# Performance work log

Measured on AMD Instinct MI355X. Metric: run time of the kernel, lower is better.

The kernel has to match this reference:

```python
import jax, jax.numpy as jnp
import numpy as np

N_NODES = 100000
N_EDGES = 1600000


def _lin_init(k, din, dout):
    # xavier-normal-ish weight, zero bias handled separately
    s = (2.0 / (din + dout)) ** 0.5
    return jax.random.normal(k, (din, dout), jnp.float32) * s


def setup_inputs() -> dict:
    key = jax.random.key(0)
    ks = jax.random.split(key, 32)
    inp = {
        "node_feat": jax.random.normal(ks[0], (N_NODES, 3), jnp.float32),
        "edge_feat": jax.random.normal(ks[1], (N_EDGES, 1), jnp.float32),
        "edge_dist": jax.random.normal(ks[2], (N_EDGES, 1), jnp.float32),
        "src": jax.random.randint(ks[3], (N_EDGES,), 0, N_NODES),
        "dst": jax.random.randint(ks[4], (N_EDGES,), 0, N_NODES),
    }
    dims = {"enc": [3, 64, 64, 8], "dec": [8, 64, 64, 1],
            "nod": [9, 64, 64, 8], "edg": [17, 64, 64, 1]}
    i = 5
    for name, d in dims.items():
        for l in range(3):
            inp[f"w_{name}{l+1}"] = _lin_init(ks[i], d[l], d[l + 1]); i += 1
            inp[f"b_{name}{l+1}"] = jnp.zeros((d[l + 1],), jnp.float32)
    return inp


def _mlp(x, w1, b1, w2, b2, w3, b3):
    x = jax.nn.relu(x @ w1 + b1)
    x = jax.nn.relu(x @ w2 + b2)
    return jax.nn.relu(x @ w3 + b3)


def _edge_softmax(dist, dst, n):
    # softmax over incoming edges per destination node (DGL edge_softmax)
    m = jax.ops.segment_max(dist, dst, num_segments=n)          # [N,1]
    e = jnp.exp(dist - m[dst])                                   # [E,1]
    s = jax.ops.segment_sum(e, dst, num_segments=n)              # [N,1]
    return e / s[dst]


def reference(node_feat, edge_feat, edge_dist, src, dst,
              w_enc1, b_enc1, w_enc2, b_enc2, w_enc3, b_enc3,
              w_dec1, b_dec1, w_dec2, b_dec2, w_dec3, b_dec3,
              w_nod1, b_nod1, w_nod2, b_nod2, w_nod3, b_nod3,
              w_edg1, b_edg1, w_edg2, b_edg2, w_edg3, b_edg3):
    n = node_feat.shape[0]
    # encoder: [N,3] -> [N,8]
    h = _mlp(node_feat, w_enc1, b_enc1, w_enc2, b_enc2, w_enc3, b_enc3)
    # softmax-weighted aggregation of src features to dst
    w = _edge_softmax(edge_dist, dst, n)                         # [E,1]
    h = jax.ops.segment_sum(w * h[src], dst, num_segments=n)     # [N,8]
    he = edge_feat                                               # [E,1]
    for _ in range(2):
        x = jnp.concatenate([he, h[src], h[dst]], axis=-1)       # [E,17]
        he = _mlp(x, w_edg1, b_edg1, w_edg2, b_edg2, w_edg3, b_edg3)  # [E,1]
        agg = jax.ops.segment_sum(he, dst, num_segments=n)       # [N,1]
        h = _mlp(jnp.concatenate([agg, h], axis=-1),
                 w_nod1, b_nod1, w_nod2, b_nod2, w_nod3, b_nod3)  # [N,8]
    # second softmax aggregation (same dist -> same weights)
    h = jax.ops.segment_sum(w * h[src], dst, num_segments=n)     # [N,8]
    # decoder: [N,8] -> [N,1]
    return _mlp(h, w_dec1, b_dec1, w_dec2, b_dec2, w_dec3, b_dec3)
```

## Files before the change

### kernel.cpp

```cpp
#include <hip/hip_runtime.h>

#define N_NODES 100000
#define N_EDGES 1600000

typedef __attribute__((ext_vector_type(4))) float f32x4;
typedef __attribute__((ext_vector_type(8))) short bf16x8;

__device__ __forceinline__ unsigned short f2bf(float v) {
    unsigned u = __float_as_uint(v);
    unsigned r = (u + 0x7FFFu + ((u >> 16) & 1u)) >> 16;
    return (unsigned short)r;
}
__device__ __forceinline__ float bf2f(unsigned short h) {
    return __uint_as_float(((unsigned)h) << 16);
}

__global__ void zero_kernel(float* p, int n) {
    int i = blockIdx.x * blockDim.x + threadIdx.x;
    int stride = gridDim.x * blockDim.x;
    for (; i < n; i += stride) p[i] = 0.f;
}

__global__ void exp_sum_kernel(const float* __restrict__ dist, const int* __restrict__ dst,
                               float* __restrict__ s, float* __restrict__ wbuf, int E) {
    int e = blockIdx.x * blockDim.x + threadIdx.x;
    if (e >= E) return;
    float v = expf(dist[e]);
    wbuf[e] = v;
    atomicAdd(s + dst[e], v);
}

template <bool NORM>
__global__ void agg_kernel(float* wbuf, const float* __restrict__ s,
                           const float* __restrict__ hfeat,
                           const int* __restrict__ src, const int* __restrict__ dst,
                           float* __restrict__ out, int E) {
    int t = blockIdx.x * blockDim.x + threadIdx.x;
    if (t >= E * 8) return;
    int e = t >> 3, c = t & 7;
    float w = wbuf[e];
    int d = dst[e];
    if (NORM) {
        w = w / s[d];
        if (c == 0) wbuf[e] = w;
    }
    atomicAdd(out + d * 8 + c, w * hfeat[src[e] * 8 + c]);
}

struct PackArgs { const float *w1, *b1, *w2; float* out; int din, stride; };

__global__ void pack_kernel(PackArgs a0, PackArgs a1, PackArgs a2) {
    PackArgs a = (blockIdx.x == 0) ? a0 : (blockIdx.x == 1) ? a1 : a2;
    int k = threadIdx.x;
    float* row = a.out + k * a.stride;
    for (int j = 0; j < 64; ++j) row[j] = a.w2[k * 64 + j];
    for (int j = 0; j < a.din; ++j) row[64 + j] = a.w1[j * 64 + k];
    row[64 + a.din] = a.b1[k];
}

__global__ void pack_edge_kernel(const float* __restrict__ w1, const float* __restrict__ w2,
                                 unsigned short* __restrict__ w1hi, unsigned short* __restrict__ w1lo,
                                 unsigned short* __restrict__ w2hi, unsigned short* __restrict__ w2lo) {
    int c = threadIdx.x;
    for (int j = 0; j < 32; ++j) {
        float v = (j < 17) ? w1[j * 64 + c] : 0.f;
        unsigned short hi = f2bf(v);
        w1hi[c * 32 + j] = hi;
        w1lo[c * 32 + j] = f2bf(v - bf2f(hi));
    }
    int mt = c >> 4, row = c & 15;
    for (int ch = 0; ch < 64; ++ch) {
        int ks = ch >> 5, r5 = ch & 31;
        int i = ((r5 >> 4) << 2) | (r5 & 3);
        int g = (r5 >> 2) & 3;
        int dstIdx = (((mt * 2 + ks) * 16 + row) * 4 + g) * 8 + i;
        float v = w2[ch * 64 + c];
        unsigned short hi = f2bf(v);
        w2hi[dstIdx] = hi;
        w2lo[dstIdx] = f2bf(v - bf2f(hi));
    }
}

template <int DIN, int DOUT, int STRIDE>
__device__ __forceinline__ void mlp_fused(
    const float* __restrict__ x, const float* __restrict__ wp,
    const float* __restrict__ b2,
    const float* __restrict__ w3, const float* __restrict__ b3,
    float* __restrict__ out) {
    float h2[64];
#pragma unroll
    for (int j = 0; j < 64; ++j) h2[j] = b2[j];
    for (int k = 0; k < 64; ++k) {
        const float* row = wp + k * STRIDE;
        float a = row[64 + DIN];
#pragma unroll
        for (int j = 0; j < DIN; ++j) a = fmaf(x[j], row[64 + j], a);
        a = fmaxf(a, 0.f);
#pragma unroll
        for (int j = 0; j < 64; ++j) h2[j] = fmaf(a, row[j], h2[j]);
    }
    float acc[DOUT];
#pragma unroll
    for (int o = 0; o < DOUT; ++o) acc[o] = b3[o];
#pragma unroll
    for (int j = 0; j < 64; ++j) {
        float r = fmaxf(h2[j], 0.f);
#pragma unroll
        for (int o = 0; o < DOUT; ++o) acc[o] = fmaf(r, w3[j * DOUT + o], acc[o]);
    }
#pragma unroll
    for (int o = 0; o < DOUT; ++o) out[o] = fmaxf(acc[o], 0.f);
}

template <int CA, int CB, int DOUT, int STRIDE>
__global__ __launch_bounds__(256, 3) void node_mlp_kernel(
    const float* __restrict__ xa, const float* __restrict__ xb,
    const float* __restrict__ wp, const float* __restrict__ b2,
    const float* __restrict__ w3, const float* __restrict__ b3,
    float* __restrict__ out, int n) {
    constexpr int DIN = CA + CB;
    int i = blockIdx.x * 256 + threadIdx.x;
    if (i >= n) return;
    float x[DIN];
#pragma unroll
    for (int k = 0; k < CA; ++k) x[k] = xa[i * CA + k];
    if (CB == 8) {
        float4 v0 = *(const float4*)(xb + i * 8);
        float4 v1 = *(const float4*)(xb + i * 8 + 4);
        x[CA + 0] = v0.x; x[CA + 1] = v0.y; x[CA + 2] = v0.z; x[CA + 3] = v0.w;
        x[CA + 4] = v1.x; x[CA + 5] = v1.y; x[CA + 6] = v1.z; x[CA + 7] = v1.w;
    }
    float o[DOUT];
    mlp_fused<DIN, DOUT, STRIDE>(x, wp, b2, w3, b3, o);
#pragma unroll
    for (int k = 0; k < DOUT; ++k) out[i * DOUT + k] = o[k];
}

__global__ __launch_bounds__(128, 2) void edge_mlp_mfma_kernel(
    const float* __restrict__ he_in, const float* __restrict__ h,
    const int* __restrict__ src, const int* __restrict__ dst,
    const unsigned short* __restrict__ w1hi, const unsigned short* __restrict__ w1lo,
    const unsigned short* __restrict__ w2hi, const unsigned short* __restrict__ w2lo,
    const float* __restrict__ b1, const float* __restrict__ b2,
    const float* __restrict__ w3, const float* __restrict__ b3,
    float* __restrict__ he_out, float* __restrict__ agg) {
    __shared__ __align__(16) unsigned char smem[2 * 10240];
    const int lane = threadIdx.x & 63, wv = threadIdx.x >> 6;
    unsigned char* W = smem + wv * 10240;
    const int ebase = (blockIdx.x * 2 + wv) * 64;

    {
        int e = ebase + lane;
        float x[32];
        x[0] = he_in[e];
        int sr = src[e], dd = dst[e];
        float4 a0 = *(const float4*)(h + sr * 8);
        float4 a1 = *(const float4*)(h + sr * 8 + 4);
        float4 d0 = *(const float4*)(h + dd * 8);
        float4 d1 = *(const float4*)(h + dd * 8 + 4);
        x[1] = a0.x;  x[2] = a0.y;  x[3] = a0.z;  x[4] = a0.w;
        x[5] = a1.x;  x[6] = a1.y;  x[7] = a1.z;  x[8] = a1.w;
        x[9] = d0.x;  x[10] = d0.y; x[11] = d0.z; x[12] = d0.w;
        x[13] = d1.x; x[14] = d1.y; x[15] = d1.z; x[16] = d1.w;
#pragma unroll
        for (int j = 17; j < 32; ++j) x[j] = 0.f;
        unsigned uh[16], ul[16];
#pragma unroll
        for (int jj = 0; jj < 16; ++jj) {
            unsigned short h0 = f2bf(x[2 * jj]);
            unsigned short h1v = f2bf(x[2 * jj + 1]);
            unsigned short l0 = f2bf(x[2 * jj] - bf2f(h0));
            unsigned short l1 = f2bf(x[2 * jj + 1] - bf2f(h1v));
            uh[jj] = (unsigned)h0 | ((unsigned)h1v << 16);
            ul[jj] = (unsigned)l0 | ((unsigned)l1 << 16);
        }
        uint4* ph = (uint4*)(W + lane * 80);
        uint4* pl = (uint4*)(W + 5120 + lane * 80);
#pragma unroll
        for (int q = 0; q < 4; ++q) {
            ph[q] = make_uint4(uh[4 * q], uh[4 * q + 1], uh[4 * q + 2], uh[4 * q + 3]);
            pl[q] = make_uint4(ul[4 * q], ul[4 * q + 1], ul[4 * q + 2], ul[4 * q + 3]);
        }
    }
    __syncthreads();
    const int row = lane & 15, g = lane >> 4;

    bf16x8 wa_h[4], wa_l[4];
#pragma unroll
    for (int mt = 0; mt < 4; ++mt) {
        wa_h[mt] = *(const bf16x8*)(w1hi + (16 * mt + row) * 32 + g * 8);
        wa_l[mt] = *(const bf16x8*)(w1lo + (16 * mt + row) * 32 + g * 8);
    }
    bf16x8 xb_h[4], xb_l[4];
#pragma unroll
    for (int nt = 0; nt < 4; ++nt) {
        xb_h[nt] = *(const bf16x8*)(W + (16 * nt + row) * 80 + g * 16);
        xb_l[nt] = *(const bf16x8*)(W + 5120 + (16 * nt + row) * 80 + g * 16);
    }
    f32x4 c1[4][4];
#pragma unroll
    for (int mt = 0; mt < 4; ++mt)
#pragma unroll
        for (int nt = 0; nt < 4; ++nt) {
            f32x4 c = {0.f, 0.f, 0.f, 0.f};
            c = __builtin_amdgcn_mfma_f32_16x16x32_bf16(wa_h[mt], xb_h[nt], c, 0, 0, 0);
            c = __builtin_amdgcn_mfma_f32_16x16x32_bf16(wa_h[mt], xb_l[nt], c, 0, 0, 0);
            c = __builtin_amdgcn_mfma_f32_16x16x32_bf16(wa_l[mt], xb_h[nt], c, 0, 0, 0);
            c1[mt][nt] = c;
        }

    float4 b1v[4];
#pragma unroll
    for (int mt = 0; mt < 4; ++mt) b1v[mt] = *(const float4*)(b1 + 16 * mt + g * 4);
    bf16x8 pb_h[4][2], pb_l[4][2];
#pragma unroll
    for (int nt = 0; nt < 4; ++nt)
#pragma unroll
        for (int ks = 0; ks < 2; ++ks) {
            float v0 = fmaxf(c1[2 * ks][nt].x + b1v[2 * ks].x, 0.f);
            float v1 = fmaxf(c1[2 * ks][nt].y + b1v[2 * ks].y, 0.f);
            float v2 = fmaxf(c1[2 * ks][nt].z + b1v[2 * ks].z, 0.f);
            float v3 = fmaxf(c1[2 * ks][nt].w + b1v[2 * ks].w, 0.f);
            float v4 = fmaxf(c1[2 * ks + 1][nt].x + b1v[2 * ks + 1].x, 0.f);
            float v5 = fmaxf(c1[2 * ks + 1][nt].y + b1v[2 * ks + 1].y, 0.f);
            float v6 = fmaxf(c1[2 * ks + 1][nt].z + b1v[2 * ks + 1].z, 0.f);
            float v7 = fmaxf(c1[2 * ks + 1][nt].w + b1v[2 * ks + 1].w, 0.f);
            unsigned short h0 = f2bf(v0), h1v = f2bf(v1), h2v = f2bf(v2), h3 = f2bf(v3);
            unsigned short h4 = f2bf(v4), h5 = f2bf(v5), h6 = f2bf(v6), h7 = f2bf(v7);
            bf16x8 ph, pl;
            ph[0] = h0; ph[1] = h1v; ph[2] = h2v; ph[3] = h3;
            ph[4] = h4; ph[5] = h5;  ph[6] = h6;  ph[7] = h7;
            pl[0] = f2bf(v0 - bf2f(h0)); pl[1] = f2bf(v1 - bf2f(h1v));
            pl[2] = f2bf(v2 - bf2f(h2v)); pl[3] = f2bf(v3 - bf2f(h3));
            pl[4] = f2bf(v4 - bf2f(h4)); pl[5] = f2bf(v5 - bf2f(h5));
            pl[6] = f2bf(v6 - bf2f(h6)); pl[7] = f2bf(v7 - bf2f(h7));
            pb_h[nt][ks] = ph;
            pb_l[nt][ks] = pl;
        }

    f32x4 c2[4][4];
#pragma unroll
    for (int mt = 0; mt < 4; ++mt)
#pragma unroll
        for (int nt = 0; nt < 4; ++nt) c2[mt][nt] = (f32x4){0.f, 0.f, 0.f, 0.f};
#pragma unroll
    for (int mt = 0; mt < 4; ++mt) {
        bf16x8 w2a_h[2], w2a_l[2];
#pragma unroll
        for (int ks = 0; ks < 2; ++ks) {
            int off = (((mt * 2 + ks) * 16 + row) * 4 + g) * 8;
            w2a_h[ks] = *(const bf16x8*)(w2hi + off);
            w2a_l[ks] = *(const bf16x8*)(w2lo + off);
        }
#pragma unroll
        for (int nt = 0; nt < 4; ++nt)
#pragma unroll
            for (int ks = 0; ks < 2; ++ks) {
                c2[mt][nt] = __builtin_amdgcn_mfma_f32_16x16x32_bf16(w2a_h[ks], pb_h[nt][ks], c2[mt][nt], 0, 0, 0);
                c2[mt][nt] = __builtin_amdgcn_mfma_f32_16x16x32_bf16(w2a_h[ks], pb_l[nt][ks], c2[mt][nt], 0, 0, 0);
                c2[mt][nt] = __builtin_amdgcn_mfma_f32_16x16x32_bf16(w2a_l[ks], pb_h[nt][ks], c2[mt][nt], 0, 0, 0);
            }
    }

    float4 b2v[4], w3v[4];
#pragma unroll
    for (int mt = 0; mt < 4; ++mt) {
        b2v[mt] = *(const float4*)(b2 + 16 * mt + g * 4);
        w3v[mt] = *(const float4*)(w3 + 16 * mt + g * 4);
    }
    float b3s = b3[0];
    float pacc[4];
#pragma unroll
    for (int nt = 0; nt < 4; ++nt) {
        float p = 0.f;
#pragma unroll
        for (int mt = 0; mt < 4; ++mt) {
            p = fmaf(fmaxf(c2[mt][nt].x + b2v[mt].x, 0.f), w3v[mt].x, p);
            p = fmaf(fmaxf(c2[mt][nt].y + b2v[mt].y, 0.f), w3v[mt].y, p);
            p = fmaf(fmaxf(c2[mt][nt].z + b2v[mt].z, 0.f), w3v[mt].z, p);
            p = fmaf(fmaxf(c2[mt][nt].w + b2v[mt].w, 0.f), w3v[mt].w, p);
        }
        p += __shfl_xor(p, 16);
        p += __shfl_xor(p, 32);
        pacc[nt] = p;
    }
    if (lane < 16) {
#pragma unroll
        for (int nt = 0; nt < 4; ++nt) {
            int e2 = ebase + 16 * nt + lane;
            float o = fmaxf(pacc[nt] + b3s, 0.f);
            he_out[e2] = o;
            atomicAdd(agg + dst[e2], o);
        }
    }
}

extern "C" void kernel_launch(void* const* d_in, const int* in_sizes, int n_in,
                              void* d_out, int out_size, void* d_ws, size_t ws_size,
                              hipStream_t stream) {
    const int N = N_NODES, E = N_EDGES;
    const float* node_feat = (const float*)d_in[0];
    const float* edge_feat = (const float*)d_in[1];
    const float* edge_dist = (const float*)d_in[2];
    const int* src = (const int*)d_in[3];
    const int* dst = (const int*)d_in[4];
    const float* w_enc1 = (const float*)d_in[5];  const float* b_enc1 = (const float*)d_in[6];
    const float* w_enc2 = (const float*)d_in[7];  const float* b_enc2 = (const float*)d_in[8];
    const float* w_enc3 = (const float*)d_in[9];  const float* b_enc3 = (const float*)d_in[10];
    const float* w_dec1 = (const float*)d_in[11]; const float* b_dec1 = (const float*)d_in[12];
    const float* w_dec2 = (const float*)d_in[13]; const float* b_dec2 = (const float*)d_in[14];
    const float* w_dec3 = (const float*)d_in[15]; const float* b_dec3 = (const float*)d_in[16];
    const float* w_nod1 = (const float*)d_in[17]; const float* b_nod1 = (const float*)d_in[18];
    const float* w_nod2 = (const float*)d_in[19]; const float* b_nod2 = (const float*)d_in[20];
    const float* w_nod3 = (const float*)d_in[21]; const float* b_nod3 = (const float*)d_in[22];
    const float* w_edg1 = (const float*)d_in[23]; const float* b_edg1 = (const float*)d_in[24];
    const float* w_edg2 = (const float*)d_in[25]; const float* b_edg2 = (const float*)d_in[26];
    const float* w_edg3 = (const float*)d_in[27]; const float* b_edg3 = (const float*)d_in[28];

    float* ws = (float*)d_ws;
    float* s      = ws;
    float* hagg1  = ws + N;
    float* agg1   = ws + 9 * N;
    float* agg2   = ws + 10 * N;
    float* hagg2  = ws + 11 * N;
    float* h_enc  = ws + 19 * N;
    float* h_r1   = ws + 27 * N;
    float* h_r2   = ws + 35 * N;
    float* wbuf   = ws + 43 * N;
    float* he1    = wbuf + E;
    float* he2    = he1 + E;
    float* pk_enc = he2 + E;
    float* pk_nod = pk_enc + 64 * 80;
    float* pk_dec = pk_nod + 64 * 80;
    unsigned short* w1hi = (unsigned short*)(pk_dec + 64 * 80);
    unsigned short* w1lo = w1hi + 64 * 32;
    unsigned short* w2hi = w1lo + 64 * 32;
    unsigned short* w2lo = w2hi + 64 * 64;

    PackArgs pa0{w_enc1, b_enc1, w_enc2, pk_enc, 3, 80};
    PackArgs pa1{w_nod1, b_nod1, w_nod2, pk_nod, 9, 80};
    PackArgs pa2{w_dec1, b_dec1, w_dec2, pk_dec, 8, 80};
    pack_kernel<<<3, 64, 0, stream>>>(pa0, pa1, pa2);
    pack_edge_kernel<<<1, 64, 0, stream>>>(w_edg1, w_edg2, w1hi, w1lo, w2hi, w2lo);

    zero_kernel<<<2048, 256, 0, stream>>>(ws, 19 * N);
    node_mlp_kernel<3, 0, 8, 80><<<(N + 255) / 256, 256, 0, stream>>>(node_feat, nullptr,
        pk_enc, b_enc2, w_enc3, b_enc3, h_enc, N);
    exp_sum_kernel<<<(E + 255) / 256, 256, 0, stream>>>(edge_dist, dst, s, wbuf, E);
    agg_kernel<true><<<(E * 8 + 255) / 256, 256, 0, stream>>>(wbuf, s, h_enc, src, dst, hagg1, E);
    edge_mlp_mfma_kernel<<<E / 128, 128, 0, stream>>>(edge_feat, hagg1, src, dst,
        w1hi, w1lo, w2hi, w2lo, b_edg1, b_edg2, w_edg3, b_edg3, he1, agg1);
    node_mlp_kernel<1, 8, 8, 80><<<(N + 255) / 256, 256, 0, stream>>>(agg1, hagg1,
        pk_nod, b_nod2, w_nod3, b_nod3, h_r1, N);
    edge_mlp_mfma_kernel<<<E / 128, 128, 0, stream>>>(he1, h_r1, src, dst,
        w1hi, w1lo, w2hi, w2lo, b_edg1, b_edg2, w_edg3, b_edg3, he2, agg2);
    node_mlp_kernel<1, 8, 8, 80><<<(N + 255) / 256, 256, 0, stream>>>(agg2, h_r1,
        pk_nod, b_nod2, w_nod3, b_nod3, h_r2, N);
    agg_kernel<false><<<(E * 8 + 255) / 256, 256, 0, stream>>>(wbuf, s, h_r2, src, dst, hagg2, E);
    node_mlp_kernel<8, 0, 1, 80><<<(N + 255) / 256, 256, 0, stream>>>(hagg2, nullptr,
        pk_dec, b_dec2, w_dec3, b_dec3, (float*)d_out, N);
}
```

Baseline: 721.4 us.

## Build edge MLP B-fragments directly in registers, skipping LDS staging

The edge MLP kernel no longer gathers each edge's 17-feature input into shared memory and reads it back as MFMA fragments. Each lane now gathers its own 8-wide slice (src features, dst features, or the edge scalar) straight into bf16 hi/lo fragment registers. The first-layer weight packing is permuted to match this K ordering. The block grows to 4 waves of 256 threads with no LDS or barrier, and f2bf switches to the HIP intrinsic. The cost is more redundant gather loads per lane, since each edge row is loaded across four nt iterations by different lane groups, and possibly higher register pressure.

```diff
diff --git a/kernel.cpp b/kernel.cpp
--- a/kernel.cpp
+++ b/kernel.cpp
@@ -1,4 +1,5 @@
 #include <hip/hip_runtime.h>
+#include <hip/hip_bf16.h>
 
 #define N_NODES 100000
 #define N_EDGES 1600000
@@ -7,9 +8,7 @@
 typedef __attribute__((ext_vector_type(8))) short bf16x8;
 
 __device__ __forceinline__ unsigned short f2bf(float v) {
-    unsigned u = __float_as_uint(v);
-    unsigned r = (u + 0x7FFFu + ((u >> 16) & 1u)) >> 16;
-    return (unsigned short)r;
+    return __builtin_bit_cast(unsigned short, __float2bfloat16(v));
 }
 __device__ __forceinline__ float bf2f(unsigned short h) {
     return __uint_as_float(((unsigned)h) << 16);
@@ -62,11 +61,11 @@
                                  unsigned short* __restrict__ w1hi, unsigned short* __restrict__ w1lo,
                                  unsigned short* __restrict__ w2hi, unsigned short* __restrict__ w2lo) {
     int c = threadIdx.x;
-    for (int j = 0; j < 32; ++j) {
-        float v = (j < 17) ? w1[j * 64 + c] : 0.f;
+    for (int k = 0; k < 32; ++k) {
+        float v = (k < 16) ? w1[(k + 1) * 64 + c] : (k == 16 ? w1[c] : 0.f);
         unsigned short hi = f2bf(v);
-        w1hi[c * 32 + j] = hi;
-        w1lo[c * 32 + j] = f2bf(v - bf2f(hi));
+        w1hi[c * 32 + k] = hi;
+        w1lo[c * 32 + k] = f2bf(v - bf2f(hi));
     }
     int mt = c >> 4, row = c & 15;
     for (int ch = 0; ch < 64; ++ch) {
@@ -136,7 +135,7 @@
     for (int k = 0; k < DOUT; ++k) out[i * DOUT + k] = o[k];
 }
 
-__global__ __launch_bounds__(128, 2) void edge_mlp_mfma_kernel(
+__global__ __launch_bounds__(256) void edge_mlp_mfma_kernel(
     const float* __restrict__ he_in, const float* __restrict__ h,
     const int* __restrict__ src, const int* __restrict__ dst,
     const unsigned short* __restrict__ w1hi, const unsigned short* __restrict__ w1lo,
@@ -144,58 +143,42 @@
     const float* __restrict__ b1, const float* __restrict__ b2,
     const float* __restrict__ w3, const float* __restrict__ b3,
     float* __restrict__ he_out, float* __restrict__ agg) {
-    __shared__ __align__(16) unsigned char smem[2 * 10240];
     const int lane = threadIdx.x & 63, wv = threadIdx.x >> 6;
-    unsigned char* W = smem + wv * 10240;
-    const int ebase = (blockIdx.x * 2 + wv) * 64;
-
-    {
-        int e = ebase + lane;
-        float x[32];
-        x[0] = he_in[e];
-        int sr = src[e], dd = dst[e];
-        float4 a0 = *(const float4*)(h + sr * 8);
-        float4 a1 = *(const float4*)(h + sr * 8 + 4);
-        float4 d0 = *(const float4*)(h + dd * 8);
-        float4 d1 = *(const float4*)(h + dd * 8 + 4);
-        x[1] = a0.x;  x[2] = a0.y;  x[3] = a0.z;  x[4] = a0.w;
-        x[5] = a1.x;  x[6] = a1.y;  x[7] = a1.z;  x[8] = a1.w;
-        x[9] = d0.x;  x[10] = d0.y; x[11] = d0.z; x[12] = d0.w;
-        x[13] = d1.x; x[14] = d1.y; x[15] = d1.z; x[16] = d1.w;
-#pragma unroll
-        for (int j = 17; j < 32; ++j) x[j] = 0.f;
-        unsigned uh[16], ul[16];
-#pragma unroll
-        for (int jj = 0; jj < 16; ++jj) {
-            unsigned short h0 = f2bf(x[2 * jj]);
-            unsigned short h1v = f2bf(x[2 * jj + 1]);
-            unsigned short l0 = f2bf(x[2 * jj] - bf2f(h0));
-            unsigned short l1 = f2bf(x[2 * jj + 1] - bf2f(h1v));
-            uh[jj] = (unsigned)h0 | ((unsigned)h1v << 16);
-            ul[jj] = (unsigned)l0 | ((unsigned)l1 << 16);
-        }
-        uint4* ph = (uint4*)(W + lane * 80);
-        uint4* pl = (uint4*)(W + 5120 + lane * 80);
-#pragma unroll
-        for (int q = 0; q < 4; ++q) {
-            ph[q] = make_uint4(uh[4 * q], uh[4 * q + 1], uh[4 * q + 2], uh[4 * q + 3]);
-            pl[q] = make_uint4(ul[4 * q], ul[4 * q + 1], ul[4 * q + 2], ul[4 * q + 3]);
-        }
-    }
-    __syncthreads();
+    const int ebase = (blockIdx.x * 4 + wv) * 64;
     const int row = lane & 15, g = lane >> 4;
+
+    bf16x8 xb_h[4], xb_l[4];
+#pragma unroll
+    for (int nt = 0; nt < 4; ++nt) {
+        int e = ebase + 16 * nt + row;
+        float v[8];
+        if (g < 2) {
+            int n = (g == 0) ? src[e] : dst[e];
+            float4 A = *(const float4*)(h + n * 8);
+            float4 B = *(const float4*)(h + n * 8 + 4);
+            v[0] = A.x; v[1] = A.y; v[2] = A.z; v[3] = A.w;
+            v[4] = B.x; v[5] = B.y; v[6] = B.z; v[7] = B.w;
+        } else {
+            v[0] = (g == 2) ? he_in[e] : 0.f;
+            v[1] = 0.f; v[2] = 0.f; v[3] = 0.f;
+            v[4] = 0.f; v[5] = 0.f; v[6] = 0.f; v[7] = 0.f;
+        }
+        bf16x8 hv, lv;
+#pragma unroll
+        for (int j = 0; j < 8; ++j) {
+            unsigned short hb = f2bf(v[j]);
+            hv[j] = (short)hb;
+            lv[j] = (short)f2bf(v[j] - bf2f(hb));
+        }
+        xb_h[nt] = hv;
+        xb_l[nt] = lv;
+    }
 
     bf16x8 wa_h[4], wa_l[4];
 #pragma unroll
     for (int mt = 0; mt < 4; ++mt) {
         wa_h[mt] = *(const bf16x8*)(w1hi + (16 * mt + row) * 32 + g * 8);
         wa_l[mt] = *(const bf16x8*)(w1lo + (16 * mt + row) * 32 + g * 8);
-    }
-    bf16x8 xb_h[4], xb_l[4];
-#pragma unroll
-    for (int nt = 0; nt < 4; ++nt) {
-        xb_h[nt] = *(const bf16x8*)(W + (16 * nt + row) * 80 + g * 16);
-        xb_l[nt] = *(const bf16x8*)(W + 5120 + (16 * nt + row) * 80 + g * 16);
     }
     f32x4 c1[4][4];
 #pragma unroll
@@ -348,11 +331,11 @@
         pk_enc, b_enc2, w_enc3, b_enc3, h_enc, N);
     exp_sum_kernel<<<(E + 255) / 256, 256, 0, stream>>>(edge_dist, dst, s, wbuf, E);
     agg_kernel<true><<<(E * 8 + 255) / 256, 256, 0, stream>>>(wbuf, s, h_enc, src, dst, hagg1, E);
-    edge_mlp_mfma_kernel<<<E / 128, 128, 0, stream>>>(edge_feat, hagg1, src, dst,
+    edge_mlp_mfma_kernel<<<E / 256, 256, 0, stream>>>(edge_feat, hagg1, src, dst,
         w1hi, w1lo, w2hi, w2lo, b_edg1, b_edg2, w_edg3, b_edg3, he1, agg1);
     node_mlp_kernel<1, 8, 8, 80><<<(N + 255) / 256, 256, 0, stream>>>(agg1, hagg1,
         pk_nod, b_nod2, w_nod3, b_nod3, h_r1, N);
-    edge_mlp_mfma_kernel<<<E / 128, 128, 0, stream>>>(he1, h_r1, src, dst,
+    edge_mlp_mfma_kernel<<<E / 256, 256, 0, stream>>>(he1, h_r1, src, dst,
         w1hi, w1lo, w2hi, w2lo, b_edg1, b_edg2, w_edg3, b_edg3, he2, agg2);
     node_mlp_kernel<1, 8, 8, 80><<<(N + 255) / 256, 256, 0, stream>>>(agg2, h_r1,
         pk_nod, b_nod2, w_nod3, b_nod3, h_r2, N);
```

New measurement: 751.8 us. 1.04x slower.

## Fuse edge softmax with first aggregation and defer normalization to per-node scale

Applied to the files above, without the earlier changes.

Merges the exp/sum pass and the first weighted aggregation into one per-edge kernel that accumulates unnormalized exp-weighted features. The softmax division moves to a per-node normalization pass, and for the second aggregation to a scale applied when the decoder loads its input. This drops one full edge pass and the per-edge division, and replaces 8-threads-per-edge gathers with one thread per edge doing float4 loads. The trade is more atomics issued per thread. Skipping the max subtraction was already the case before, so overflow risk is unchanged. The bf16 conversion helper also switches to the library intrinsic.

```diff
diff --git a/kernel.cpp b/kernel.cpp
--- a/kernel.cpp
+++ b/kernel.cpp
@@ -1,4 +1,5 @@
 #include <hip/hip_runtime.h>
+#include <hip/hip_bf16.h>
 
 #define N_NODES 100000
 #define N_EDGES 1600000
@@ -7,9 +8,7 @@
 typedef __attribute__((ext_vector_type(8))) short bf16x8;
 
 __device__ __forceinline__ unsigned short f2bf(float v) {
-    unsigned u = __float_as_uint(v);
-    unsigned r = (u + 0x7FFFu + ((u >> 16) & 1u)) >> 16;
-    return (unsigned short)r;
+    return __builtin_bit_cast(unsigned short, __float2bfloat16(v));
 }
 __device__ __forceinline__ float bf2f(unsigned short h) {
     return __uint_as_float(((unsigned)h) << 16);
@@ -21,30 +20,54 @@
     for (; i < n; i += stride) p[i] = 0.f;
 }
 
-__global__ void exp_sum_kernel(const float* __restrict__ dist, const int* __restrict__ dst,
-                               float* __restrict__ s, float* __restrict__ wbuf, int E) {
+__global__ void exp_agg_kernel(const float* __restrict__ dist,
+                               const int* __restrict__ src, const int* __restrict__ dst,
+                               const float* __restrict__ h,
+                               float* __restrict__ s, float* __restrict__ wbuf,
+                               float* __restrict__ hagg, int E) {
     int e = blockIdx.x * blockDim.x + threadIdx.x;
     if (e >= E) return;
     float v = expf(dist[e]);
     wbuf[e] = v;
-    atomicAdd(s + dst[e], v);
-}
-
-template <bool NORM>
-__global__ void agg_kernel(float* wbuf, const float* __restrict__ s,
-                           const float* __restrict__ hfeat,
-                           const int* __restrict__ src, const int* __restrict__ dst,
-                           float* __restrict__ out, int E) {
-    int t = blockIdx.x * blockDim.x + threadIdx.x;
-    if (t >= E * 8) return;
-    int e = t >> 3, c = t & 7;
-    float w = wbuf[e];
-    int d = dst[e];
-    if (NORM) {
-        w = w / s[d];
-        if (c == 0) wbuf[e] = w;
-    }
-    atomicAdd(out + d * 8 + c, w * hfeat[src[e] * 8 + c]);
+    int d = dst[e], sr = src[e];
+    atomicAdd(s + d, v);
+    float4 A = *(const float4*)(h + sr * 8);
+    float4 B = *(const float4*)(h + sr * 8 + 4);
+    float* o = hagg + d * 8;
+    atomicAdd(o + 0, v * A.x); atomicAdd(o + 1, v * A.y);
+    atomicAdd(o + 2, v * A.z); atomicAdd(o + 3, v * A.w);
+    atomicAdd(o + 4, v * B.x); atomicAdd(o + 5, v * B.y);
+    atomicAdd(o + 6, v * B.z); atomicAdd(o + 7, v * B.w);
+}
+
+__global__ void agg2_kernel(const float* __restrict__ wbuf, const float* __restrict__ h,
+                            const int* __restrict__ src, const int* __restrict__ dst,
+                            float* __restrict__ out, int E) {
+    int e = blockIdx.x * blockDim.x + threadIdx.x;
+    if (e >= E) return;
+    float v = wbuf[e];
+    int d = dst[e], sr = src[e];
+    float4 A = *(const float4*)(h + sr * 8);
+    float4 B = *(const float4*)(h + sr * 8 + 4);
+    float* o = out + d * 8;
+    atomicAdd(o + 0, v * A.x); atomicAdd(o + 1, v * A.y);
+    atomicAdd(o + 2, v * A.z); atomicAdd(o + 3, v * A.w);
+    atomicAdd(o + 4, v * B.x); atomicAdd(o + 5, v * B.y);
+    atomicAdd(o + 6, v * B.z); atomicAdd(o + 7, v * B.w);
+}
+
+__global__ void norm_kernel(float* __restrict__ hagg, const float* __restrict__ s,
+                            float* __restrict__ rs, int N) {
+    int d = blockIdx.x * blockDim.x + threadIdx.x;
+    if (d >= N) return;
+    float r = 1.f / s[d];
+    rs[d] = r;
+    float4 a = *(const float4*)(hagg + d * 8);
+    float4 b = *(const float4*)(hagg + d * 8 + 4);
+    a.x *= r; a.y *= r; a.z *= r; a.w *= r;
+    b.x *= r; b.y *= r; b.z *= r; b.w *= r;
+    *(float4*)(hagg + d * 8) = a;
+    *(float4*)(hagg + d * 8 + 4) = b;
 }
 
 struct PackArgs { const float *w1, *b1, *w2; float* out; int din, stride; };
@@ -115,15 +138,17 @@
 template <int CA, int CB, int DOUT, int STRIDE>
 __global__ __launch_bounds__(256, 3) void node_mlp_kernel(
     const float* __restrict__ xa, const float* __restrict__ xb,
+    const float* __restrict__ rs,
     const float* __restrict__ wp, const float* __restrict__ b2,
     const float* __restrict__ w3, const float* __restrict__ b3,
     float* __restrict__ out, int n) {
     constexpr int DIN = CA + CB;
     int i = blockIdx.x * 256 + threadIdx.x;
     if (i >= n) return;
+    float scale = rs ? rs[i] : 1.f;
     float x[DIN];
 #pragma unroll
-    for (int k = 0; k < CA; ++k) x[k] = xa[i * CA + k];
+    for (int k = 0; k < CA; ++k) x[k] = xa[i * CA + k] * scale;
     if (CB == 8) {
         float4 v0 = *(const float4*)(xb + i * 8);
         float4 v1 = *(const float4*)(xb + i * 8 + 4);
@@ -323,10 +348,11 @@
     float* agg1   = ws + 9 * N;
     float* agg2   = ws + 10 * N;
     float* hagg2  = ws + 11 * N;
-    float* h_enc  = ws + 19 * N;
-    float* h_r1   = ws + 27 * N;
-    float* h_r2   = ws + 35 * N;
-    float* wbuf   = ws + 43 * N;
+    float* rs     = ws + 19 * N;
+    float* h_enc  = ws + 20 * N;
+    float* h_r1   = ws + 28 * N;
+    float* h_r2   = ws + 36 * N;
+    float* wbuf   = ws + 44 * N;
     float* he1    = wbuf + E;
     float* he2    = he1 + E;
     float* pk_enc = he2 + E;
@@ -345,18 +371,19 @@
 
     zero_kernel<<<2048, 256, 0, stream>>>(ws, 19 * N);
     node_mlp_kernel<3, 0, 8, 80><<<(N + 255) / 256, 256, 0, stream>>>(node_feat, nullptr,
-        pk_enc, b_enc2, w_enc3, b_enc3, h_enc, N);
-    exp_sum_kernel<<<(E + 255) / 256, 256, 0, stream>>>(edge_dist, dst, s, wbuf, E);
-    agg_kernel<true><<<(E * 8 + 255) / 256, 256, 0, stream>>>(wbuf, s, h_enc, src, dst, hagg1, E);
+        nullptr, pk_enc, b_enc2, w_enc3, b_enc3, h_enc, N);
+    exp_agg_kernel<<<(E + 255) / 256, 256, 0, stream>>>(edge_dist, src, dst, h_enc,
+        s, wbuf, hagg1, E);
+    norm_kernel<<<(N + 255) / 256, 256, 0, stream>>>(hagg1, s, rs, N);
     edge_mlp_mfma_kernel<<<E / 128, 128, 0, stream>>>(edge_feat, hagg1, src, dst,
         w1hi, w1lo, w2hi, w2lo, b_edg1, b_edg2, w_edg3, b_edg3, he1, agg1);
     node_mlp_kernel<1, 8, 8, 80><<<(N + 255) / 256, 256, 0, stream>>>(agg1, hagg1,
-        pk_nod, b_nod2, w_nod3, b_nod3, h_r1, N);
+        nullptr, pk_nod, b_nod2, w_nod3, b_nod3, h_r1, N);
     edge_mlp_mfma_kernel<<<E / 128, 128, 0, stream>>>(he1, h_r1, src, dst,
         w1hi, w1lo, w2hi, w2lo, b_edg1, b_edg2, w_edg3, b_edg3, he2, agg2);
     node_mlp_kernel<1, 8, 8, 80><<<(N + 255) / 256, 256, 0, stream>>>(agg2, h_r1,
-        pk_nod, b_nod2, w_nod3, b_nod3, h_r2, N);
-    agg_kernel<false><<<(E * 8 + 255) / 256, 256, 0, stream>>>(wbuf, s, h_r2, src, dst, hagg2, E);
+        nullptr, pk_nod, b_nod2, w_nod3, b_nod3, h_r2, N);
+    agg2_kernel<<<(E + 255) / 256, 256, 0, stream>>>(wbuf, h_r2, src, dst, hagg2, E);
     node_mlp_kernel<8, 0, 1, 80><<<(N + 255) / 256, 256, 0, stream>>>(hagg2, nullptr,
-        pk_dec, b_dec2, w_dec3, b_dec3, (float*)d_out, N);
-}
+        rs, pk_dec, b_dec2, w_dec3, b_dec3, (float*)d_out, N);
+}
```

Measured after the change: 1.851 ms. 157% more time.
